# Kernel optimization log

Hardware: AMD Instinct MI355X
Metric: run time of the kernel (lower is better)

## Reference

```python
import jax, jax.numpy as jnp
import numpy as np

N = 512          # number of grid nodes (len(x))
BATCH = 128
AMPLITUDE = 0.1  # diffusion coefficient k


def setup_inputs() -> dict:
    key = jax.random.key(0)
    forcing = jax.random.normal(key, (BATCH, N), dtype=jnp.float32)
    return {"forcing_functions": forcing}


def _assemble(forcing):
    # forcing: [B, n]
    B, n = forcing.shape
    h = 1.0 / (n - 1)
    c = AMPLITUDE / h
    # Element loop assembles tridiagonal K: diag 2c interior, -c off-diags.
    main = jnp.full((n,), 2.0 * c, dtype=jnp.float32).at[0].set(1.0).at[-1].set(1.0)
    # Dirichlet BC zeroes row/col 0 and n-1, so first/last off-diagonal entries vanish.
    off = jnp.full((n - 1,), -c, dtype=jnp.float32).at[0].set(0.0).at[-1].set(0.0)
    K = jnp.diag(main) + jnp.diag(off, 1) + jnp.diag(off, -1)  # [n, n]
    # Load vector: two hat basis functions evaluated at 0.5 sum to 1 -> f*h/2.
    u_left = jnp.sin(jnp.float32(jnp.pi) * jnp.float32(0.0))   # sin(0) = 0
    u_right = jnp.sin(jnp.float32(jnp.pi) * jnp.float32(1.0))  # sin(pi) in fp32
    f = jnp.zeros((B, n), dtype=jnp.float32)
    f = f.at[:, 1:-1].set(forcing[:, 1:-1] * jnp.float32(h / 2.0))
    f = f.at[:, 0].set(u_left).at[:, -1].set(u_right)
    return K, f


def reference(forcing_functions):
    K, f = _assemble(forcing_functions)
    # K is identical across the batch -> one multi-RHS solve (same math as the
    # original batched torch.linalg.solve with replicated K).
    sol = jnp.linalg.solve(K, f.T).T  # [B, n]
    return sol
```

## Files before the change

### kernel.cpp

```cpp
#include <hip/hip_runtime.h>


#define NN   512
#define BATCH 128

__global__ __launch_bounds__(NN) void darcy_solve_kernel(
    const float* __restrict__ forcing, float* __restrict__ out) {
    __shared__ float sA[NN];
    __shared__ float sC[NN];

    const int b = blockIdx.x;
    const int t = threadIdx.x;

    const float scale = (float)((1.0 / 511.0) * (1.0 / 511.0) / 0.2);

    const float fval = forcing[b * NN + t];
    const float g = (t >= 1 && t <= NN - 2) ? fval * scale : 0.0f;

    sA[t] = (float)t * g;
    sC[t] = (float)(NN - 1 - t) * g;
    __syncthreads();

    #pragma unroll
    for (int off = 1; off < NN; off <<= 1) {
        float va = 0.0f, vc = 0.0f;
        if (t >= off) { va = sA[t - off]; vc = sC[t - off]; }
        __syncthreads();
        sA[t] += va;
        sC[t] += vc;
        __syncthreads();
    }

    const float ctot = sC[NN - 1];

    float u;
    if (t == 0) {
        u = 0.0f;
    } else if (t == NN - 1) {
        u = -8.7422777e-08f;
    } else {
        const float s1 = sA[t];
        const float s2 = ctot - sC[t];
        u = ((float)(NN - 1 - t) * s1 + (float)t * s2) * (1.0f / 511.0f);
    }
    out[b * NN + t] = u;
}

extern "C" void kernel_launch(void* const* d_in, const int* in_sizes, int n_in,
                              void* d_out, int out_size, void* d_ws, size_t ws_size,
                              hipStream_t stream) {
    const float* forcing = (const float*)d_in[0];
    float* out = (float*)d_out;
    darcy_solve_kernel<<<dim3(BATCH), dim3(NN), 0, stream>>>(forcing, out);
}
```

Before: 53.43 us.

## Replace block-wide shared-memory scan with single-wavefront register scan

Each row is now handled by one 64-lane wavefront, and each lane owns 8 contiguous elements loaded and stored as float4. Each lane runs a serial prefix sum over its 8 elements, then a wavefront shuffle scan combines the lane totals. This removes the 9-step shared-memory Hillis-Steele scan and its barriers. It also changes the order of the floating-point additions, so results may differ slightly in rounding.

```diff
diff --git a/kernel.cpp b/kernel.cpp
--- a/kernel.cpp
+++ b/kernel.cpp
@@ -1,49 +1,59 @@
 #include <hip/hip_runtime.h>
 
 
-#define NN   512
+#define NN    512
 #define BATCH 128
 
-__global__ __launch_bounds__(NN) void darcy_solve_kernel(
+__global__ __launch_bounds__(64) void darcy_wave_kernel(
     const float* __restrict__ forcing, float* __restrict__ out) {
-    __shared__ float sA[NN];
-    __shared__ float sC[NN];
-
-    const int b = blockIdx.x;
-    const int t = threadIdx.x;
+    const int b    = blockIdx.x;
+    const int lane = threadIdx.x;
+    const int base = lane * 8;
 
     const float scale = (float)((1.0 / 511.0) * (1.0 / 511.0) / 0.2);
 
-    const float fval = forcing[b * NN + t];
-    const float g = (t >= 1 && t <= NN - 2) ? fval * scale : 0.0f;
+    const float4* fp = (const float4*)(forcing + b * NN + base);
+    const float4 f0 = fp[0];
+    const float4 f1 = fp[1];
+    const float f[8] = {f0.x, f0.y, f0.z, f0.w, f1.x, f1.y, f1.z, f1.w};
 
-    sA[t] = (float)t * g;
-    sC[t] = (float)(NN - 1 - t) * g;
-    __syncthreads();
-
-    #pragma unroll
-    for (int off = 1; off < NN; off <<= 1) {
-        float va = 0.0f, vc = 0.0f;
-        if (t >= off) { va = sA[t - off]; vc = sC[t - off]; }
-        __syncthreads();
-        sA[t] += va;
-        sC[t] += vc;
-        __syncthreads();
+    float pa[8], pc[8];
+    float ra = 0.0f, rc = 0.0f;
+#pragma unroll
+    for (int i = 0; i < 8; ++i) {
+        const int j = base + i;
+        const float g = (j >= 1 && j <= NN - 2) ? f[i] * scale : 0.0f;
+        ra += (float)j * g;
+        rc += (float)(NN - 1 - j) * g;
+        pa[i] = ra;
+        pc[i] = rc;
     }
 
-    const float ctot = sC[NN - 1];
+    float sa = ra, sc = rc;
+#pragma unroll
+    for (int off = 1; off < 64; off <<= 1) {
+        const float ua = __shfl_up(sa, off, 64);
+        const float uc = __shfl_up(sc, off, 64);
+        if (lane >= off) { sa += ua; sc += uc; }
+    }
+    const float offA = sa - ra;
+    const float offC = sc - rc;
+    const float ctot = __shfl(sc, 63, 64);
 
-    float u;
-    if (t == 0) {
-        u = 0.0f;
-    } else if (t == NN - 1) {
-        u = -8.7422777e-08f;
-    } else {
-        const float s1 = sA[t];
-        const float s2 = ctot - sC[t];
-        u = ((float)(NN - 1 - t) * s1 + (float)t * s2) * (1.0f / 511.0f);
+    float o[8];
+#pragma unroll
+    for (int i = 0; i < 8; ++i) {
+        const int j  = base + i;
+        const float PA = offA + pa[i];
+        const float PC = offC + pc[i];
+        o[i] = ((float)(NN - 1 - j) * PA + (float)j * (ctot - PC)) * (1.0f / 511.0f);
     }
-    out[b * NN + t] = u;
+    if (lane == 0)  o[0] = 0.0f;
+    if (lane == 63) o[7] = -8.7422777e-08f;
+
+    float4* op = (float4*)(out + b * NN + base);
+    op[0] = make_float4(o[0], o[1], o[2], o[3]);
+    op[1] = make_float4(o[4], o[5], o[6], o[7]);
 }
 
 extern "C" void kernel_launch(void* const* d_in, const int* in_sizes, int n_in,
@@ -51,5 +61,5 @@
                               hipStream_t stream) {
     const float* forcing = (const float*)d_in[0];
     float* out = (float*)d_out;
-    darcy_solve_kernel<<<dim3(BATCH), dim3(NN), 0, stream>>>(forcing, out);
+    darcy_wave_kernel<<<dim3(BATCH), dim3(64), 0, stream>>>(forcing, out);
 }
```

Measured after the change: 52.64 us. No clear change (-1.5%).
